# Kernel optimization log

Hardware: AMD Instinct MI355X
Metric: run time of the kernel (lower is better)

Reference implementation:

```python
import jax, jax.numpy as jnp
import numpy as np

N = 100000   # nodes
E = 1600000  # edges (avg degree 16)
D = 64       # in_channels
OUT = 64     # out_channels


def setup_inputs() -> dict:
    key = jax.random.key(0)
    k1, k2, k3, k4, k5 = jax.random.split(key, 5)
    x = jax.random.normal(k1, (N, D), jnp.float32)
    edge_index = jax.random.randint(k2, (2, E), 0, N, dtype=jnp.int32)
    x0 = jax.random.normal(k3, (N, D), jnp.float32)
    W_weight = jax.random.normal(k4, (OUT, D), jnp.float32) * (1.0 / np.sqrt(D))
    W_bias = jax.random.normal(k5, (OUT,), jnp.float32) * 0.01
    return {"x": x, "edge_index": edge_index, "x0": x0,
            "W_weight": W_weight, "W_bias": W_bias}


def reference(x, edge_index, x0, W_bias, W_weight):
    n = x.shape[0]
    # gcn_norm with add_self_loops=True (PyG default), improved=False
    self_loops = jnp.arange(n, dtype=edge_index.dtype)
    row = jnp.concatenate([edge_index[0], self_loops])  # source nodes
    col = jnp.concatenate([edge_index[1], self_loops])  # target nodes
    w = jnp.ones(row.shape[0], dtype=x.dtype)
    deg = jax.ops.segment_sum(w, col, num_segments=n)   # in-degree (+1 self loop)
    deg_inv_sqrt = jnp.where(deg > 0, jax.lax.rsqrt(jnp.maximum(deg, 1e-12)), 0.0)
    norm = deg_inv_sqrt[row] * deg_inv_sqrt[col]        # [E+N]
    # SpMM: adj_t = SparseTensor(row=col, col=row) -> out[c] = sum_e norm_e * x[row_e]
    agg = jax.ops.segment_sum(x[row] * norm[:, None], col, num_segments=n)  # [N, D]
    # use_init=False, use_weight=True -> trailing Linear
    return agg @ W_weight.T + W_bias
```

## Files before the change

### kernel.cpp

```cpp
#include <hip/hip_runtime.h>


#define NBMAX 400
#define CAP   5120

typedef short bf16x8 __attribute__((ext_vector_type(8)));
typedef float f32x4  __attribute__((ext_vector_type(4)));

__device__ inline float bflo(unsigned u) { return __uint_as_float(u << 16); }
__device__ inline float bfhi(unsigned u) { return __uint_as_float(u & 0xFFFF0000u); }
__device__ inline unsigned short f2bf(float f) {
    unsigned u = __float_as_uint(f);
    u += 0x7FFFu + ((u >> 16) & 1u);
    return (unsigned short)(u >> 16);
}

__device__ inline void acc8(float* a, float4 v) {
    unsigned x = __float_as_uint(v.x), y = __float_as_uint(v.y);
    unsigned z = __float_as_uint(v.z), w = __float_as_uint(v.w);
    a[0] += bflo(x); a[1] += bfhi(x); a[2] += bflo(y); a[3] += bfhi(y);
    a[4] += bflo(z); a[5] += bfhi(z); a[6] += bflo(w); a[7] += bfhi(w);
}

__global__ void k_initcur(int* __restrict__ gcur, int NB) {
    int b = threadIdx.x;
    if (b < NB) gcur[b] = b * CAP;
}

__global__ __launch_bounds__(256) void k_bin(const int* __restrict__ row,
                                             const int* __restrict__ col,
                                             int* __restrict__ gcur,
                                             unsigned int* __restrict__ ebuf, int E) {
    __shared__ unsigned int   sorted4[4096];
    __shared__ unsigned short sbkt[4096];
    __shared__ int h[NBMAX], hstart[NBMAX], hcur[NBMAX], gof[NBMAX];
    int t = threadIdx.x;
    int base = blockIdx.x * 4096;
    int total = min(4096, E - base);

    int rr[16], cc[16];
    #pragma unroll
    for (int i = 0; i < 4; ++i) {
        int e0 = (t + i * 256) * 4;
        if (e0 + 3 < total) {
            int4 r4 = *(const int4*)(row + base + e0);
            int4 c4 = *(const int4*)(col + base + e0);
            rr[i*4+0]=r4.x; rr[i*4+1]=r4.y; rr[i*4+2]=r4.z; rr[i*4+3]=r4.w;
            cc[i*4+0]=c4.x; cc[i*4+1]=c4.y; cc[i*4+2]=c4.z; cc[i*4+3]=c4.w;
        } else {
            #pragma unroll
            for (int j = 0; j < 4; ++j) {
                int e = e0 + j;
                if (e < total) { rr[i*4+j] = row[base+e]; cc[i*4+j] = col[base+e]; }
                else cc[i*4+j] = -1;
            }
        }
    }
    for (int b = t; b < NBMAX; b += 256) h[b] = 0;
    __syncthreads();
    #pragma unroll
    for (int i = 0; i < 16; ++i)
        if (cc[i] >= 0) atomicAdd(&h[cc[i] >> 8], 1);
    __syncthreads();
    if (t < 64) {
        int lo = t * 7;
        int loc[7]; int s = 0;
        #pragma unroll
        for (int i = 0; i < 7; ++i) {
            loc[i] = s;
            int idx = lo + i;
            s += (idx < NBMAX) ? h[idx] : 0;
        }
        int incl = s;
        for (int off = 1; off < 64; off <<= 1) {
            int v = __shfl_up(incl, off);
            if (t >= off) incl += v;
        }
        int ex = incl - s;
        #pragma unroll
        for (int i = 0; i < 7; ++i) {
            int idx = lo + i;
            if (idx < NBMAX) hstart[idx] = ex + loc[i];
        }
    }
    __syncthreads();
    for (int b = t; b < NBMAX; b += 256) hcur[b] = hstart[b];
    __syncthreads();
    #pragma unroll
    for (int i = 0; i < 16; ++i) {
        if (cc[i] >= 0) {
            int b = cc[i] >> 8;
            int rank = atomicAdd(&hcur[b], 1);
            sorted4[rank] = (unsigned)rr[i] | ((unsigned)(cc[i] & 255) << 24);
            sbkt[rank] = (unsigned short)b;
        }
    }
    for (int b = t; b < NBMAX; b += 256) {
        int m = h[b];
        gof[b] = m ? atomicAdd(&gcur[b], m) : 0;
    }
    __syncthreads();
    for (int i = t; i < total; i += 256) {
        int b = sbkt[i];
        ebuf[gof[b] + (i - hstart[b])] = sorted4[i];
    }
}

__global__ __launch_bounds__(256) void k_cnt(const unsigned int* __restrict__ ebuf,
                                             const int* __restrict__ gcur,
                                             float* __restrict__ dinv, int n) {
    __shared__ int h[256];
    int b = blockIdx.x, t = threadIdx.x;
    int s0 = b * CAP;
    int count = min(gcur[b] - s0, CAP);
    h[t] = 0;
    __syncthreads();
    for (int i = t; i < count; i += 256) atomicAdd(&h[ebuf[s0 + i] >> 24], 1);
    __syncthreads();
    int c = b * 256 + t;
    if (c < n) dinv[c] = rsqrtf((float)(h[t] + 1));
}

__global__ __launch_bounds__(256) void k_gemm(const float* __restrict__ x,
                                              const float* __restrict__ W,
                                              const float* __restrict__ dinv,
                                              unsigned short* __restrict__ yb, int n) {
    __shared__ __align__(16) unsigned short xs[64][72];
    __shared__ __align__(16) unsigned short Wb[64][72];
    int t = threadIdx.x;
    long long total = (long long)n * 64;
    long long xbase = (long long)blockIdx.x * 4096;
    #pragma unroll
    for (int i = 0; i < 4; ++i) {
        int idx = t + i * 256;
        int r = idx >> 4, c4 = (idx & 15) << 2;
        long long g = xbase + (long long)idx * 4;
        float4 v;
        if (g + 3 < total) v = *(const float4*)(x + g);
        else {
            v.x = (g + 0 < total) ? x[g + 0] : 0.f;
            v.y = (g + 1 < total) ? x[g + 1] : 0.f;
            v.z = (g + 2 < total) ? x[g + 2] : 0.f;
            v.w = (g + 3 < total) ? x[g + 3] : 0.f;
        }
        ushort4 o; o.x = f2bf(v.x); o.y = f2bf(v.y); o.z = f2bf(v.z); o.w = f2bf(v.w);
        *(ushort4*)&xs[r][c4] = o;
        float4 wv = *(const float4*)(W + idx * 4);
        ushort4 wo; wo.x = f2bf(wv.x); wo.y = f2bf(wv.y); wo.z = f2bf(wv.z); wo.w = f2bf(wv.w);
        *(ushort4*)&Wb[r][c4] = wo;
    }
    __syncthreads();
    int lane = t & 63, wid = t >> 6;
    int m  = wid * 16 + (lane & 15);
    int kg = (lane >> 4) * 8;
    bf16x8 a0 = *(bf16x8*)&xs[m][kg];
    bf16x8 a1 = *(bf16x8*)&xs[m][32 + kg];
    int bn = lane & 15;
    f32x4 acc0 = {0.f,0.f,0.f,0.f}, acc1 = acc0, acc2 = acc0, acc3 = acc0;
    {
        bf16x8 b0 = *(bf16x8*)&Wb[bn][kg], b1 = *(bf16x8*)&Wb[bn][32 + kg];
        acc0 = __builtin_amdgcn_mfma_f32_16x16x32_bf16(a0, b0, acc0, 0, 0, 0);
        acc0 = __builtin_amdgcn_mfma_f32_16x16x32_bf16(a1, b1, acc0, 0, 0, 0);
    }
    {
        bf16x8 b0 = *(bf16x8*)&Wb[bn + 16][kg], b1 = *(bf16x8*)&Wb[bn + 16][32 + kg];
        acc1 = __builtin_amdgcn_mfma_f32_16x16x32_bf16(a0, b0, acc1, 0, 0, 0);
        acc1 = __builtin_amdgcn_mfma_f32_16x16x32_bf16(a1, b1, acc1, 0, 0, 0);
    }
    {
        bf16x8 b0 = *(bf16x8*)&Wb[bn + 32][kg], b1 = *(bf16x8*)&Wb[bn + 32][32 + kg];
        acc2 = __builtin_amdgcn_mfma_f32_16x16x32_bf16(a0, b0, acc2, 0, 0, 0);
        acc2 = __builtin_amdgcn_mfma_f32_16x16x32_bf16(a1, b1, acc2, 0, 0, 0);
    }
    {
        bf16x8 b0 = *(bf16x8*)&Wb[bn + 48][kg], b1 = *(bf16x8*)&Wb[bn + 48][32 + kg];
        acc3 = __builtin_amdgcn_mfma_f32_16x16x32_bf16(a0, b0, acc3, 0, 0, 0);
        acc3 = __builtin_amdgcn_mfma_f32_16x16x32_bf16(a1, b1, acc3, 0, 0, 0);
    }
    int rbase = blockIdx.x * 64 + wid * 16 + (lane >> 4) * 4;
    #pragma unroll
    for (int i = 0; i < 4; ++i) {
        int r = rbase + i;
        if (r < n) {
            float dv = dinv[r];
            long long ro = (long long)r * 64 + (lane & 15);
            yb[ro +  0] = f2bf(dv * acc0[i]);
            yb[ro + 16] = f2bf(dv * acc1[i]);
            yb[ro + 32] = f2bf(dv * acc2[i]);
            yb[ro + 48] = f2bf(dv * acc3[i]);
        }
    }
}

__global__ __launch_bounds__(1024) void k_aggr(const unsigned int* __restrict__ ebuf,
                                               const int* __restrict__ gcur,
                                               const float* __restrict__ dinv,
                                               const unsigned short* __restrict__ yb,
                                               const float* __restrict__ bias,
                                               float* __restrict__ out, int n) {
    __shared__ int h[256], hstart[256], hc[256], wsum[4];
    __shared__ int rnk[256], slotmap[256];
    __shared__ int sbuf[CAP];
    int b = blockIdx.x, t = threadIdx.x;
    int s0 = b * CAP;
    int count = min(gcur[b] - s0, CAP);

    if (t < 256) { h[t] = 0; rnk[t] = 0; }
    __syncthreads();
    unsigned rec[5];
    #pragma unroll
    for (int k = 0; k < 5; ++k) {
        int i = t + k * 1024;
        if (i < count) {
            unsigned p = ebuf[s0 + i];
            rec[k] = p;
            atomicAdd(&h[p >> 24], 1);
        }
    }
    __syncthreads();
    if (t < 256) {
        int v = h[t];
        int lane = t & 63, wid = t >> 6;
        int incl = v;
        #pragma unroll
        for (int off = 1; off < 64; off <<= 1) {
            int u = __shfl_up(incl, off);
            if (lane >= off) incl += u;
        }
        hstart[t] = incl;
        if (lane == 63) wsum[wid] = incl;
    }
    {
        int cl2 = t & 255, part = t >> 8;
        int lt = h[cl2];
        int base2 = part << 6;
        int rk = 0;
        for (int u2 = base2; u2 < base2 + 64; ++u2) {
            int lu = h[u2];
            rk += ((lu > lt) || (lu == lt && u2 < cl2)) ? 1 : 0;
        }
        if (rk) atomicAdd(&rnk[cl2], rk);
    }
    __syncthreads();
    if (t < 256) {
        int wid = t >> 6;
        int add = 0;
        for (int w = 0; w < wid; ++w) add += wsum[w];
        int ex = hstart[t] - h[t] + add;
        hstart[t] = ex;
        hc[t] = ex;
        slotmap[rnk[t]] = t;
    }
    __syncthreads();
    #pragma unroll
    for (int k = 0; k < 5; ++k) {
        int i = t + k * 1024;
        if (i < count) {
            unsigned p = rec[k];
            int r = atomicAdd(&hc[p >> 24], 1);
            sbuf[r] = (int)(p & 0x1FFFFu);
        }
    }
    __syncthreads();

    int lane = t & 63, w = t >> 6;
    int g = lane >> 3, q = lane & 7;
    int qo = q << 3;
    #pragma unroll 1
    for (int r = 0; r < 2; ++r) {
        int slot = w * 8 + g;
        int cl = slotmap[r == 0 ? slot : 255 - slot];
        int c = b * 256 + cl;
        if (c >= n) continue;
        int start = hstart[cl], len = h[cl];
        float sa[8] = {0.f,0.f,0.f,0.f,0.f,0.f,0.f,0.f};
        float ua[8] = {0.f,0.f,0.f,0.f,0.f,0.f,0.f,0.f};
        float4 vself = *(const float4*)(yb + (long long)c * 64 + qo);
        int i = 0;
        for (; i + 4 <= len; i += 4) {
            int e0 = sbuf[start + i + 0];
            int e1 = sbuf[start + i + 1];
            int e2 = sbuf[start + i + 2];
            int e3 = sbuf[start + i + 3];
            float4 v0 = *(const float4*)(yb + (long long)e0 * 64 + qo);
            float4 v1 = *(const float4*)(yb + (long long)e1 * 64 + qo);
            float4 v2 = *(const float4*)(yb + (long long)e2 * 64 + qo);
            float4 v3 = *(const float4*)(yb + (long long)e3 * 64 + qo);
            acc8(sa, v0); acc8(ua, v1); acc8(sa, v2); acc8(ua, v3);
        }
        for (; i < len; ++i) {
            int e0 = sbuf[start + i];
            float4 v0 = *(const float4*)(yb + (long long)e0 * 64 + qo);
            acc8(sa, v0);
        }
        acc8(ua, vself);
        float dc = dinv[c];
        float4 b0 = *(const float4*)(bias + qo);
        float4 b1 = *(const float4*)(bias + qo + 4);
        float4 o0 = make_float4(dc * (sa[0] + ua[0]) + b0.x,
                                dc * (sa[1] + ua[1]) + b0.y,
                                dc * (sa[2] + ua[2]) + b0.z,
                                dc * (sa[3] + ua[3]) + b0.w);
        float4 o1 = make_float4(dc * (sa[4] + ua[4]) + b1.x,
                                dc * (sa[5] + ua[5]) + b1.y,
                                dc * (sa[6] + ua[6]) + b1.z,
                                dc * (sa[7] + ua[7]) + b1.w);
        *(float4*)(out + (long long)c * 64 + qo)     = o0;
        *(float4*)(out + (long long)c * 64 + qo + 4) = o1;
    }
}

extern "C" void kernel_launch(void* const* d_in, const int* in_sizes, int n_in,
                              void* d_out, int out_size, void* d_ws, size_t ws_size,
                              hipStream_t stream) {
    const float* x    = (const float*)d_in[0];
    const int*   ei   = (const int*)d_in[1];
    const float* W    = (const float*)d_in[3];
    const float* bias = (const float*)d_in[4];
    float* out = (float*)d_out;

    int n = in_sizes[0] / 64;
    int E = in_sizes[1] / 2;
    const int* row = ei;
    const int* col = ei + E;

    int NB = (n + 255) / 256;

    char* ws = (char*)d_ws;
    size_t off = 0;
    auto alloc = [&](size_t bytes) { char* p = ws + off; off += (bytes + 15) & ~size_t(15); return p; };
    int*            gcur = (int*)  alloc((size_t)NB * 4);
    float*          dinv = (float*)alloc((size_t)n * 4);
    unsigned short* yb   = (unsigned short*)alloc((size_t)n * 64 * 2);
    unsigned int*   ebuf = (unsigned int*)alloc((size_t)NB * CAP * 4);

    int nbE = (E + 4095) / 4096;

    k_initcur<<<1, 512, 0, stream>>>(gcur, NB);
    k_bin <<<nbE, 256, 0, stream>>>(row, col, gcur, ebuf, E);
    k_cnt <<<NB, 256, 0, stream>>>(ebuf, gcur, dinv, n);
    k_gemm<<<(n + 63) / 64, 256, 0, stream>>>(x, W, dinv, yb, n);
    k_aggr<<<NB, 1024, 0, stream>>>(ebuf, gcur, dinv, yb, bias, out, n);
}
```

Baseline: 178.1 us.

## Move per-bucket CSR sort into count kernel and split aggregation into smaller blocks

The count kernel now does the full per-bucket counting sort, ordering edges by target node and also by a source-index sub-key (bits 13-16) for better gather locality. It writes sorted source indices back to global memory along with per-node degree-ranked order, start and length arrays. Aggregation becomes a lightweight 256-thread kernel launched with four times as many blocks that reads this precomputed CSR, removing its shared-memory histogram, sort and big LDS buffer. The cost is extra global traffic for the sorted edges and metadata, plus a serial 256-step rank loop in the sort kernel.

New measurement: 200.2 us. +12.4%, slower.

```diff
diff --git a/kernel.cpp b/kernel.cpp
--- a/kernel.cpp
+++ b/kernel.cpp
@@ -106,19 +106,63 @@
     }
 }
 
-__global__ __launch_bounds__(256) void k_cnt(const unsigned int* __restrict__ ebuf,
-                                             const int* __restrict__ gcur,
-                                             float* __restrict__ dinv, int n) {
+__global__ __launch_bounds__(256) void k_sort(unsigned int* __restrict__ ebuf,
+                                              const int* __restrict__ gcur,
+                                              float* __restrict__ dinv,
+                                              int* __restrict__ dorder,
+                                              int* __restrict__ sstart,
+                                              int* __restrict__ slen, int n) {
+    __shared__ unsigned int sbuf[CAP];
+    __shared__ int hist[4096];
     __shared__ int h[256];
+    __shared__ int wsum[4];
     int b = blockIdx.x, t = threadIdx.x;
     int s0 = b * CAP;
     int count = min(gcur[b] - s0, CAP);
-    h[t] = 0;
-    __syncthreads();
-    for (int i = t; i < count; i += 256) atomicAdd(&h[ebuf[s0 + i] >> 24], 1);
-    __syncthreads();
+
+    for (int i = t; i < 4096; i += 256) hist[i] = 0;
+    __syncthreads();
+    for (int i = t; i < count; i += 256) {
+        unsigned p = ebuf[s0 + i];
+        sbuf[i] = p;
+        atomicAdd(&hist[((p >> 13) & 15) * 256 + (p >> 24)], 1);
+    }
+    __syncthreads();
+    int loc[16]; int s = 0;
+    #pragma unroll
+    for (int j = 0; j < 16; ++j) { loc[j] = s; s += hist[j * 256 + t]; }
+    h[t] = s;
+    int lane = t & 63, wid = t >> 6;
+    int incl = s;
+    #pragma unroll
+    for (int off = 1; off < 64; off <<= 1) {
+        int u = __shfl_up(incl, off);
+        if (lane >= off) incl += u;
+    }
+    if (lane == 63) wsum[wid] = incl;
+    __syncthreads();
+    int add = 0;
+    for (int w = 0; w < wid; ++w) add += wsum[w];
+    int ex = incl - s + add;
+    #pragma unroll
+    for (int j = 0; j < 16; ++j) hist[j * 256 + t] = ex + loc[j];
+    __syncthreads();
+    for (int i = t; i < count; i += 256) {
+        unsigned p = sbuf[i];
+        int r = atomicAdd(&hist[((p >> 13) & 15) * 256 + (p >> 24)], 1);
+        ebuf[s0 + r] = p & 0x1FFFFu;
+    }
+    int lt = h[t];
+    int rk = 0;
+    for (int u = 0; u < 256; ++u) {
+        int lu = h[u];
+        rk += ((lu > lt) || (lu == lt && u < t)) ? 1 : 0;
+    }
     int c = b * 256 + t;
-    if (c < n) dinv[c] = rsqrtf((float)(h[t] + 1));
+    dorder[b * 256 + rk] = c;
+    sstart[b * 256 + rk] = s0 + ex;
+    slen  [b * 256 + rk] = lt;
+    if (c < n) dinv[c] = rsqrtf((float)(lt + 1));
 }
 
 __global__ __launch_bounds__(256) void k_gemm(const float* __restrict__ x,
@@ -192,96 +236,33 @@
     }
 }
 
-__global__ __launch_bounds__(1024) void k_aggr(const unsigned int* __restrict__ ebuf,
-                                               const int* __restrict__ gcur,
-                                               const float* __restrict__ dinv,
-                                               const unsigned short* __restrict__ yb,
-                                               const float* __restrict__ bias,
-                                               float* __restrict__ out, int n) {
-    __shared__ int h[256], hstart[256], hc[256], wsum[4];
-    __shared__ int rnk[256], slotmap[256];
-    __shared__ int sbuf[CAP];
-    int b = blockIdx.x, t = threadIdx.x;
-    int s0 = b * CAP;
-    int count = min(gcur[b] - s0, CAP);
-
-    if (t < 256) { h[t] = 0; rnk[t] = 0; }
-    __syncthreads();
-    unsigned rec[5];
-    #pragma unroll
-    for (int k = 0; k < 5; ++k) {
-        int i = t + k * 1024;
-        if (i < count) {
-            unsigned p = ebuf[s0 + i];
-            rec[k] = p;
-            atomicAdd(&h[p >> 24], 1);
-        }
-    }
-    __syncthreads();
-    if (t < 256) {
-        int v = h[t];
-        int lane = t & 63, wid = t >> 6;
-        int incl = v;
-        #pragma unroll
-        for (int off = 1; off < 64; off <<= 1) {
-            int u = __shfl_up(incl, off);
-            if (lane >= off) incl += u;
-        }
-        hstart[t] = incl;
-        if (lane == 63) wsum[wid] = incl;
-    }
-    {
-        int cl2 = t & 255, part = t >> 8;
-        int lt = h[cl2];
-        int base2 = part << 6;
-        int rk = 0;
-        for (int u2 = base2; u2 < base2 + 64; ++u2) {
-            int lu = h[u2];
-            rk += ((lu > lt) || (lu == lt && u2 < cl2)) ? 1 : 0;
-        }
-        if (rk) atomicAdd(&rnk[cl2], rk);
-    }
-    __syncthreads();
-    if (t < 256) {
-        int wid = t >> 6;
-        int add = 0;
-        for (int w = 0; w < wid; ++w) add += wsum[w];
-        int ex = hstart[t] - h[t] + add;
-        hstart[t] = ex;
-        hc[t] = ex;
-        slotmap[rnk[t]] = t;
-    }
-    __syncthreads();
-    #pragma unroll
-    for (int k = 0; k < 5; ++k) {
-        int i = t + k * 1024;
-        if (i < count) {
-            unsigned p = rec[k];
-            int r = atomicAdd(&hc[p >> 24], 1);
-            sbuf[r] = (int)(p & 0x1FFFFu);
-        }
-    }
-    __syncthreads();
-
+__global__ __launch_bounds__(256) void k_aggr(const unsigned int* __restrict__ ssrc,
+                                              const int* __restrict__ dorder,
+                                              const int* __restrict__ sstart,
+                                              const int* __restrict__ slen,
+                                              const float* __restrict__ dinv,
+                                              const unsigned short* __restrict__ yb,
+                                              const float* __restrict__ bias,
+                                              float* __restrict__ out, int n) {
+    int t = threadIdx.x;
     int lane = t & 63, w = t >> 6;
     int g = lane >> 3, q = lane & 7;
     int qo = q << 3;
     #pragma unroll 1
     for (int r = 0; r < 2; ++r) {
-        int slot = w * 8 + g;
-        int cl = slotmap[r == 0 ? slot : 255 - slot];
-        int c = b * 256 + cl;
-        if (c >= n) continue;
-        int start = hstart[cl], len = h[cl];
+        int s = blockIdx.x * 64 + r * 32 + w * 8 + g;
+        int c = dorder[s];
+        int start = sstart[s], len = slen[s];
+        int cs = min(c, n - 1);
+        float4 vself = *(const float4*)(yb + (long long)cs * 64 + qo);
         float sa[8] = {0.f,0.f,0.f,0.f,0.f,0.f,0.f,0.f};
         float ua[8] = {0.f,0.f,0.f,0.f,0.f,0.f,0.f,0.f};
-        float4 vself = *(const float4*)(yb + (long long)c * 64 + qo);
         int i = 0;
         for (; i + 4 <= len; i += 4) {
-            int e0 = sbuf[start + i + 0];
-            int e1 = sbuf[start + i + 1];
-            int e2 = sbuf[start + i + 2];
-            int e3 = sbuf[start + i + 3];
+            int e0 = ssrc[start + i + 0];
+            int e1 = ssrc[start + i + 1];
+            int e2 = ssrc[start + i + 2];
+            int e3 = ssrc[start + i + 3];
             float4 v0 = *(const float4*)(yb + (long long)e0 * 64 + qo);
             float4 v1 = *(const float4*)(yb + (long long)e1 * 64 + qo);
             float4 v2 = *(const float4*)(yb + (long long)e2 * 64 + qo);
@@ -289,24 +270,26 @@
             acc8(sa, v0); acc8(ua, v1); acc8(sa, v2); acc8(ua, v3);
         }
         for (; i < len; ++i) {
-            int e0 = sbuf[start + i];
+            int e0 = ssrc[start + i];
             float4 v0 = *(const float4*)(yb + (long long)e0 * 64 + qo);
             acc8(sa, v0);
         }
-        acc8(ua, vself);
-        float dc = dinv[c];
-        float4 b0 = *(const float4*)(bias + qo);
-        float4 b1 = *(const float4*)(bias + qo + 4);
-        float4 o0 = make_float4(dc * (sa[0] + ua[0]) + b0.x,
-                                dc * (sa[1] + ua[1]) + b0.y,
-                                dc * (sa[2] + ua[2]) + b0.z,
-                                dc * (sa[3] + ua[3]) + b0.w);
-        float4 o1 = make_float4(dc * (sa[4] + ua[4]) + b1.x,
-                                dc * (sa[5] + ua[5]) + b1.y,
-                                dc * (sa[6] + ua[6]) + b1.z,
-                                dc * (sa[7] + ua[7]) + b1.w);
-        *(float4*)(out + (long long)c * 64 + qo)     = o0;
-        *(float4*)(out + (long long)c * 64 + qo + 4) = o1;
+        if (c < n) {
+            acc8(ua, vself);
+            float dc = dinv[c];
+            float4 b0 = *(const float4*)(bias + qo);
+            float4 b1 = *(const float4*)(bias + qo + 4);
+            float4 o0 = make_float4(dc * (sa[0] + ua[0]) + b0.x,
+                                    dc * (sa[1] + ua[1]) + b0.y,
+                                    dc * (sa[2] + ua[2]) + b0.z,
+                                    dc * (sa[3] + ua[3]) + b0.w);
+            float4 o1 = make_float4(dc * (sa[4] + ua[4]) + b1.x,
+                                    dc * (sa[5] + ua[5]) + b1.y,
+                                    dc * (sa[6] + ua[6]) + b1.z,
+                                    dc * (sa[7] + ua[7]) + b1.w);
+            *(float4*)(out + (long long)c * 64 + qo)     = o0;
+            *(float4*)(out + (long long)c * 64 + qo + 4) = o1;
+        }
     }
 }
 
@@ -329,16 +312,19 @@
     char* ws = (char*)d_ws;
     size_t off = 0;
     auto alloc = [&](size_t bytes) { char* p = ws + off; off += (bytes + 15) & ~size_t(15); return p; };
-    int*            gcur = (int*)  alloc((size_t)NB * 4);
-    float*          dinv = (float*)alloc((size_t)n * 4);
-    unsigned short* yb   = (unsigned short*)alloc((size_t)n * 64 * 2);
-    unsigned int*   ebuf = (unsigned int*)alloc((size_t)NB * CAP * 4);
+    int*            gcur   = (int*)  alloc((size_t)NB * 4);
+    float*          dinv   = (float*)alloc((size_t)n * 4);
+    unsigned short* yb     = (unsigned short*)alloc((size_t)n * 64 * 2);
+    unsigned int*   ebuf   = (unsigned int*)alloc((size_t)NB * CAP * 4);
+    int*            dorder = (int*)  alloc((size_t)NB * 256 * 4);
+    int*            sstart = (int*)  alloc((size_t)NB * 256 * 4);
+    int*            slenb  = (int*)  alloc((size_t)NB * 256 * 4);
 
     int nbE = (E + 4095) / 4096;
 
     k_initcur<<<1, 512, 0, stream>>>(gcur, NB);
     k_bin <<<nbE, 256, 0, stream>>>(row, col, gcur, ebuf, E);
-    k_cnt <<<NB, 256, 0, stream>>>(ebuf, gcur, dinv, n);
+    k_sort<<<NB, 256, 0, stream>>>(ebuf, gcur, dinv, dorder, sstart, slenb, n);
     k_gemm<<<(n + 63) / 64, 256, 0, stream>>>(x, W, dinv, yb, n);
-    k_aggr<<<NB, 1024, 0, stream>>>(ebuf, gcur, dinv, yb, bias, out, n);
-}
+    k_aggr<<<NB * 4, 256, 0, stream>>>(ebuf, dorder, sstart, slenb, dinv, yb, bias, out, n);
+}
```
